# Kernel tuning notes

Hardware: AMD Instinct MI355X
Metric: run time of the kernel (lower is better)

## Reference

```python
import jax, jax.numpy as jnp
import numpy as np

B, S, N, H, C = 32, 128, 1024, 2, 128  # batch, seq_len(=in/out channels), num_nodes, heads, out_channels
NEG_SLOPE = 0.2


def setup_inputs() -> dict:
    key = jax.random.key(0)
    k1, k2, k3, k4 = jax.random.split(key, 4)
    scale = 1.0 / np.sqrt(S)
    return {
        "x": jax.random.normal(k1, (B, S, N), dtype=jnp.float32),
        "W": jax.random.normal(k2, (H, S, C), dtype=jnp.float32) * scale,
        "att_src": jax.random.normal(k3, (H, C), dtype=jnp.float32) * scale,
        "att_dst": jax.random.normal(k4, (H, C), dtype=jnp.float32) * scale,
        "bias": jnp.zeros((C,), dtype=jnp.float32),
    }


def reference(x, W, att_src, att_dst, bias):
    # x: [B, S, N] -> node features [B, N, S]
    xt = jnp.transpose(x, (0, 2, 1))
    # per-head projection: z [B, H, N, C]
    z = jnp.einsum('bns,hsc->bhnc', xt, W)
    # scalar attention scores per node: [B, H, N]
    s_src = jnp.einsum('bhnc,hc->bhn', z, att_src)
    s_dst = jnp.einsum('bhnc,hc->bhn', z, att_dst)
    # complete graph: e[i, j] = leaky_relu(s_dst[i] + s_src[j]); softmax over sources j
    e = jax.nn.leaky_relu(s_dst[..., :, None] + s_src[..., None, :], NEG_SLOPE)
    alpha = jax.nn.softmax(e, axis=-1)  # [B, H, N, N]
    out = jnp.einsum('bhij,bhjc->bhic', alpha, z)  # [B, H, N, C]
    out = jnp.mean(out, axis=1) + bias  # concat=False -> mean over heads; [B, N, C]
    return jnp.transpose(out, (0, 2, 1))  # [B, C(=S), N]
```

## Files before the change

kernel.cpp:

```cpp
#include <hip/hip_runtime.h>
#include <hip/hip_bf16.h>
#include <math.h>

constexpr int B_ = 32, S_ = 128, N_ = 1024, H_ = 2, C_ = 128;
#define L2E_ 1.44269504088896340736f

typedef short  bf16x8 __attribute__((ext_vector_type(8)));
typedef float  f32x4  __attribute__((ext_vector_type(4)));
typedef ushort u16x8  __attribute__((ext_vector_type(8)));

__device__ __forceinline__ ushort f2bf(float f) {
    __hip_bfloat16 h = __float2bfloat16(f);
    return __builtin_bit_cast(ushort, h);
}
__device__ __forceinline__ float bfhi(ushort u) {
    return __builtin_bit_cast(float, (uint)u << 16);
}

__global__ __launch_bounds__(256)
void prep_kernel(const float* __restrict__ x, const float* __restrict__ W,
                 ushort* __restrict__ xth, ushort* __restrict__ xtl,
                 ushort* __restrict__ wth, ushort* __restrict__ wtl)
{
    __shared__ float sm[128 * 129];
    const int tid = threadIdx.x;
    const int bx = blockIdx.x;
    if (bx < 512) {
        const int b = bx >> 4, nb = (bx & 15) * 64;
        const float* xb = x + (size_t)b * S_ * N_;
#pragma unroll
        for (int it = 0; it < 32; ++it) {
            int e = it * 256 + tid;
            int s = e >> 6, n = e & 63;
            sm[s * 65 + n] = xb[(size_t)s * N_ + nb + n];
        }
        __syncthreads();
        const int n = tid >> 2, sc = (tid & 3) * 32;
        const size_t rowb = ((size_t)b * N_ + nb + n) * S_ + sc;
#pragma unroll
        for (int g = 0; g < 4; ++g) {
            u16x8 vh, vl;
#pragma unroll
            for (int e = 0; e < 8; ++e) {
                float v = sm[(sc + g * 8 + e) * 65 + n];
                ushort hh = f2bf(v);
                vh[e] = hh;
                vl[e] = f2bf(v - bfhi(hh));
            }
            *(u16x8*)&xth[rowb + g * 8] = vh;
            *(u16x8*)&xtl[rowb + g * 8] = vl;
        }
    } else {
        const int h = bx - 512;
        const float* Wh = W + (size_t)h * S_ * C_;
#pragma unroll
        for (int it = 0; it < 64; ++it) {
            int e = it * 256 + tid;
            int s = e >> 7, c = e & 127;
            sm[s * 129 + c] = Wh[s * C_ + c];
        }
        __syncthreads();
        const int c = tid >> 1, sh = (tid & 1) * 64;
        const size_t rowb = ((size_t)h * C_ + c) * S_ + sh;
#pragma unroll
        for (int g = 0; g < 8; ++g) {
            u16x8 vh, vl;
#pragma unroll
            for (int e = 0; e < 8; ++e) {
                float v = sm[(sh + g * 8 + e) * 129 + c];
                ushort hh = f2bf(v);
                vh[e] = hh;
                vl[e] = f2bf(v - bfhi(hh));
            }
            *(u16x8*)&wth[rowb + g * 8] = vh;
            *(u16x8*)&wtl[rowb + g * 8] = vl;
        }
    }
}

__global__ __launch_bounds__(256, 2)
void proj_kernel(const ushort* __restrict__ xth, const ushort* __restrict__ xtl,
                 const ushort* __restrict__ wth, const ushort* __restrict__ wtl,
                 const float* __restrict__ att_src, const float* __restrict__ att_dst,
                 ushort* __restrict__ zt, float* __restrict__ ssrc,
                 float* __restrict__ sdst)
{
    const int nb = blockIdx.x * 64;
    const int bh = blockIdx.y;
    const int b = bh >> 1, h = bh & 1;
    const int w = threadIdx.x >> 6, lane = threadIdx.x & 63;
    const int lrow = lane & 15, lq = lane >> 4;

    f32x4 acc[8];
#pragma unroll
    for (int ct = 0; ct < 8; ++ct)
#pragma unroll
        for (int r = 0; r < 4; ++r) acc[ct][r] = 0.f;

    const size_t xrow = ((size_t)b * N_ + nb + w * 16 + lrow) * S_ + lq * 8;
    const size_t wbase = (size_t)h * C_ * S_ + (size_t)lrow * S_ + lq * 8;

#pragma unroll
    for (int kc = 0; kc < 4; ++kc) {
        bf16x8 ah = *(const bf16x8*)(xth + xrow + kc * 32);
        bf16x8 al = *(const bf16x8*)(xtl + xrow + kc * 32);
#pragma unroll
        for (int ct = 0; ct < 8; ++ct) {
            const size_t wo = wbase + (size_t)ct * 16 * S_ + kc * 32;
            bf16x8 bh8 = *(const bf16x8*)(wth + wo);
            bf16x8 bl8 = *(const bf16x8*)(wtl + wo);
            acc[ct] = __builtin_amdgcn_mfma_f32_16x16x32_bf16(ah, bh8, acc[ct], 0, 0, 0);
            acc[ct] = __builtin_amdgcn_mfma_f32_16x16x32_bf16(ah, bl8, acc[ct], 0, 0, 0);
            acc[ct] = __builtin_amdgcn_mfma_f32_16x16x32_bf16(al, bh8, acc[ct], 0, 0, 0);
        }
    }

    float asrc[8], adst[8];
#pragma unroll
    for (int ct = 0; ct < 8; ++ct) {
        asrc[ct] = att_src[h * C_ + ct * 16 + lrow];
        adst[ct] = att_dst[h * C_ + ct * 16 + lrow];
    }
#pragma unroll
    for (int r = 0; r < 4; ++r) {
        float ps = 0.f, pd = 0.f;
#pragma unroll
        for (int ct = 0; ct < 8; ++ct) {
            ps = fmaf(acc[ct][r], asrc[ct], ps);
            pd = fmaf(acc[ct][r], adst[ct], pd);
        }
#pragma unroll
        for (int msk = 8; msk >= 1; msk >>= 1) {
            ps += __shfl_xor(ps, msk, 64);
            pd += __shfl_xor(pd, msk, 64);
        }
        if (lrow == 0) {
            ssrc[(size_t)bh * N_ + nb + w * 16 + lq * 4 + r] = ps;
            sdst[(size_t)bh * N_ + nb + w * 16 + lq * 4 + r] = pd;
        }
    }

#pragma unroll
    for (int ct = 0; ct < 8; ++ct) {
        ushort4 v;
        v.x = f2bf(acc[ct][0]); v.y = f2bf(acc[ct][1]);
        v.z = f2bf(acc[ct][2]); v.w = f2bf(acc[ct][3]);
        *(ushort4*)&zt[((size_t)bh * C_ + ct * 16 + lrow) * N_ + nb + w * 16 + lq * 4] = v;
    }
}

__global__ __launch_bounds__(256)
void lsum_kernel(const float* __restrict__ ssrc, const float* __restrict__ sdst,
                 float* __restrict__ caA, float* __restrict__ cbA)
{
    const int bh = blockIdx.y, ib = blockIdx.x * 256;
    const int tid = threadIdx.x;
    __shared__ float sj[N_];
    __shared__ float red[4];

    float pm = -1e30f;
#pragma unroll
    for (int it = 0; it < 4; ++it) {
        int j = it * 256 + tid;
        float v = ssrc[(size_t)bh * N_ + j] * L2E_;
        sj[j] = v;
        pm = fmaxf(pm, v);
    }
#pragma unroll
    for (int msk = 1; msk < 64; msk <<= 1) pm = fmaxf(pm, __shfl_xor(pm, msk, 64));
    if ((tid & 63) == 0) red[tid >> 6] = pm;
    __syncthreads();
    const float smax = fmaxf(fmaxf(red[0], red[1]), fmaxf(red[2], red[3]));

    const float dt = sdst[(size_t)bh * N_ + ib + tid] * L2E_;
    const float vm = dt + smax;
    const float mt = fmaxf(vm, 0.2f * vm);
    const float c1 = dt - mt, c2 = 0.2f * dt - mt;

    float l0 = 0.f, l1 = 0.f, l2 = 0.f, l3 = 0.f;
    for (int j = 0; j < N_; j += 4) {
        float4 s4 = *(const float4*)&sj[j];
        l0 += exp2f(fmaxf(s4.x + c1, fmaf(0.2f, s4.x, c2)));
        l1 += exp2f(fmaxf(s4.y + c1, fmaf(0.2f, s4.y, c2)));
        l2 += exp2f(fmaxf(s4.z + c1, fmaf(0.2f, s4.z, c2)));
        l3 += exp2f(fmaxf(s4.w + c1, fmaf(0.2f, s4.w, c2)));
    }
    const float q = log2f((l0 + l1) + (l2 + l3));
    caA[(size_t)bh * N_ + ib + tid] = c1 - q;
    cbA[(size_t)bh * N_ + ib + tid] = c2 - q;
}

__device__ __forceinline__ void stage_chunk(const ushort* __restrict__ zt, uint* zstage,
                                            int b, int w, int lane, int buf, int j0)
{
#pragma unroll
    for (int it = 0; it < 8; ++it) {
        int id = (w * 8 + it) * 64 + lane;
        int hh = id >> 10, c = (id >> 3) & 127, jq = id & 7;
        const uint* src = (const uint*)(zt + (((size_t)(b * 2 + hh) * C_ + c) * N_)
                                       + j0 + ((jq ^ (c & 7)) << 3));
        __builtin_amdgcn_global_load_lds(
            (const __attribute__((address_space(1))) uint*)src,
            (__attribute__((address_space(3))) uint*)&zstage[buf * 8192 + (w * 8 + it) * 256],
            16, 0, 0);
    }
}

__global__ __launch_bounds__(256, 1)
void attn_kernel(const ushort* __restrict__ zt, const float* __restrict__ ssrc,
                 const float* __restrict__ caA, const float* __restrict__ cbA,
                 const float* __restrict__ bias, float* __restrict__ out)
{
    const int bx = blockIdx.x;
    const int b  = blockIdx.y;
    const int tid = threadIdx.x;
    const int w = tid >> 6, lane = tid & 63;
    const int rg = w >> 1, h = w & 1;
    const int lrow = lane & 15, lq = lane >> 4;
    const int rowbase = bx * 128 + rg * 64;
    const size_t bh = (size_t)b * 2 + h;

    __shared__ uint  zstage[16384];
    __shared__ float ssjl[2][N_];

    float ca[4], cb[4], bv[8];
#pragma unroll
    for (int t = 0; t < 4; ++t) {
        ca[t] = caA[bh * N_ + rowbase + t * 16 + lrow];
        cb[t] = cbA[bh * N_ + rowbase + t * 16 + lrow];
    }
#pragma unroll
    for (int ct = 0; ct < 8; ++ct) bv[ct] = bias[ct * 16 + lrow];

#pragma unroll
    for (int it = 0; it < 8; ++it) {
        int e = it * 256 + tid;
        int hh = e >> 10, j = e & 1023;
        ssjl[hh][j] = ssrc[((size_t)b * 2 + hh) * N_ + j] * L2E_;
    }

    stage_chunk(zt, zstage, b, w, lane, 0, 0);
    __syncthreads();

    f32x4 acc[4][8];
#pragma unroll
    for (int t = 0; t < 4; ++t)
#pragma unroll
        for (int ct = 0; ct < 8; ++ct)
#pragma unroll
            for (int r = 0; r < 4; ++r) acc[t][ct][r] = 0.f;

    int buf = 0;
    for (int jc = 0; jc < 16; ++jc) {
        if (jc < 15) stage_chunk(zt, zstage, b, w, lane, buf ^ 1, (jc + 1) * 64);
#pragma unroll
        for (int ks = 0; ks < 2; ++ks) {
            const int j32 = jc * 64 + ks * 32;
            bf16x8 bf[8];
#pragma unroll
            for (int ct = 0; ct < 8; ++ct) {
                int c = ct * 16 + lrow;
                int off = buf * 32768 + h * 16384 + c * 128 + ((((ks * 4) + lq) ^ (c & 7)) << 4);
                bf[ct] = *(const bf16x8*)((const char*)zstage + off);
            }
            float4 s0 = *(const float4*)&ssjl[h][j32 + lq * 8];
            float4 s1 = *(const float4*)&ssjl[h][j32 + lq * 8 + 4];
            float sv[8] = {s0.x, s0.y, s0.z, s0.w, s1.x, s1.y, s1.z, s1.w};
#pragma unroll
            for (int t = 0; t < 4; ++t) {
                bf16x8 af;
#pragma unroll
                for (int r = 0; r < 8; ++r) {
                    float e1 = fmaxf(sv[r] + ca[t], fmaf(0.2f, sv[r], cb[t]));
                    af[r] = (short)f2bf(exp2f(e1));
                }
#pragma unroll
                for (int ct = 0; ct < 8; ++ct)
                    acc[t][ct] = __builtin_amdgcn_mfma_f32_16x16x32_bf16(af, bf[ct], acc[t][ct], 0, 0, 0);
            }
        }
        __syncthreads();
        buf ^= 1;
    }

    float* exch = (float*)zstage;
    if (h == 1) {
#pragma unroll
        for (int t = 0; t < 4; ++t)
#pragma unroll
            for (int ct = 0; ct < 8; ++ct) {
                int idx = ((((rg * 4 + t) * 8 + ct) * 16 + lrow) * 16) + lq * 4;
                *(float4*)&exch[idx] = *(float4*)&acc[t][ct];
            }
    }
    __syncthreads();
    if (h == 0) {
#pragma unroll
        for (int t = 0; t < 4; ++t)
#pragma unroll
            for (int ct = 0; ct < 8; ++ct) {
                int idx = ((((rg * 4 + t) * 8 + ct) * 16 + lrow) * 16) + lq * 4;
                float4 v = *(const float4*)&exch[idx];
                int c = ct * 16 + lrow;
                float4 o;
                o.x = 0.5f * (acc[t][ct][0] + v.x) + bv[ct];
                o.y = 0.5f * (acc[t][ct][1] + v.y) + bv[ct];
                o.z = 0.5f * (acc[t][ct][2] + v.z) + bv[ct];
                o.w = 0.5f * (acc[t][ct][3] + v.w) + bv[ct];
                *(float4*)&out[((size_t)b * C_ + c) * N_ + rowbase + t * 16 + lq * 4] = o;
            }
    }
}

extern "C" void kernel_launch(void* const* d_in, const int* in_sizes, int n_in,
                              void* d_out, int out_size, void* d_ws, size_t ws_size,
                              hipStream_t stream) {
    const float* x       = (const float*)d_in[0];
    const float* W       = (const float*)d_in[1];
    const float* att_src = (const float*)d_in[2];
    const float* att_dst = (const float*)d_in[3];
    const float* bias    = (const float*)d_in[4];
    float* out = (float*)d_out;

    ushort* xth = (ushort*)d_ws;
    ushort* xtl = xth + (size_t)B_ * N_ * S_;
    ushort* wth = xtl + (size_t)B_ * N_ * S_;
    ushort* wtl = wth + (size_t)H_ * C_ * S_;
    ushort* zt  = wtl + (size_t)H_ * C_ * S_;
    float* ssrc = (float*)(zt + (size_t)B_ * H_ * C_ * N_);
    float* sdst = ssrc + (size_t)B_ * H_ * N_;
    float* caA  = sdst + (size_t)B_ * H_ * N_;
    float* cbA  = caA + (size_t)B_ * H_ * N_;

    prep_kernel<<<dim3(514), 256, 0, stream>>>(x, W, xth, xtl, wth, wtl);
    proj_kernel<<<dim3(N_ / 64, B_ * H_), 256, 0, stream>>>(
        xth, xtl, wth, wtl, att_src, att_dst, zt, ssrc, sdst);
    lsum_kernel<<<dim3(4, B_ * H_), 256, 0, stream>>>(ssrc, sdst, caA, cbA);
    attn_kernel<<<dim3(8, B_), 256, 0, stream>>>(zt, ssrc, caA, cbA, bias, out);
}
```

Baseline: 200.6 us.

## Factor softmax exponentials, fuse x conversion into projection, restructure attention blocks

The leaky-relu softmax is rewritten so that exp(leaky(d+s)) becomes a product of precomputed per-node exponentials, selected by a threshold compare. This removes the per-element exp2 from both the row-sum loop and the attention inner loop. The x split-bf16 transpose pass is folded into the projection kernel, which now reads fp32 x directly and handles both heads per block; only W keeps a separate prep kernel. The attention kernel moves to 512 threads with a split over source columns, an XCD-aware block mapping, and a multi-wave LDS reduction before a coalesced output store. The threshold products skip max subtraction and so risk overflow or underflow for large scores.

```diff
diff --git a/kernel.cpp b/kernel.cpp
--- a/kernel.cpp
+++ b/kernel.cpp
@@ -17,229 +17,226 @@
     return __builtin_bit_cast(float, (uint)u << 16);
 }
 
-__global__ __launch_bounds__(256)
-void prep_kernel(const float* __restrict__ x, const float* __restrict__ W,
-                 ushort* __restrict__ xth, ushort* __restrict__ xtl,
-                 ushort* __restrict__ wth, ushort* __restrict__ wtl)
+__global__ __launch_bounds__(512)
+void wprep_kernel(const float* __restrict__ W,
+                  ushort* __restrict__ wth, ushort* __restrict__ wtl)
 {
     __shared__ float sm[128 * 129];
-    const int tid = threadIdx.x;
-    const int bx = blockIdx.x;
-    if (bx < 512) {
-        const int b = bx >> 4, nb = (bx & 15) * 64;
-        const float* xb = x + (size_t)b * S_ * N_;
-#pragma unroll
-        for (int it = 0; it < 32; ++it) {
-            int e = it * 256 + tid;
-            int s = e >> 6, n = e & 63;
-            sm[s * 65 + n] = xb[(size_t)s * N_ + nb + n];
-        }
-        __syncthreads();
-        const int n = tid >> 2, sc = (tid & 3) * 32;
-        const size_t rowb = ((size_t)b * N_ + nb + n) * S_ + sc;
-#pragma unroll
-        for (int g = 0; g < 4; ++g) {
-            u16x8 vh, vl;
-#pragma unroll
-            for (int e = 0; e < 8; ++e) {
-                float v = sm[(sc + g * 8 + e) * 65 + n];
-                ushort hh = f2bf(v);
-                vh[e] = hh;
-                vl[e] = f2bf(v - bfhi(hh));
-            }
-            *(u16x8*)&xth[rowb + g * 8] = vh;
-            *(u16x8*)&xtl[rowb + g * 8] = vl;
-        }
-    } else {
-        const int h = bx - 512;
-        const float* Wh = W + (size_t)h * S_ * C_;
-#pragma unroll
-        for (int it = 0; it < 64; ++it) {
-            int e = it * 256 + tid;
-            int s = e >> 7, c = e & 127;
-            sm[s * 129 + c] = Wh[s * C_ + c];
-        }
-        __syncthreads();
-        const int c = tid >> 1, sh = (tid & 1) * 64;
-        const size_t rowb = ((size_t)h * C_ + c) * S_ + sh;
-#pragma unroll
-        for (int g = 0; g < 8; ++g) {
-            u16x8 vh, vl;
-#pragma unroll
-            for (int e = 0; e < 8; ++e) {
-                float v = sm[(sh + g * 8 + e) * 129 + c];
-                ushort hh = f2bf(v);
-                vh[e] = hh;
-                vl[e] = f2bf(v - bfhi(hh));
-            }
-            *(u16x8*)&wth[rowb + g * 8] = vh;
-            *(u16x8*)&wtl[rowb + g * 8] = vl;
-        }
-    }
-}
-
-__global__ __launch_bounds__(256, 2)
-void proj_kernel(const ushort* __restrict__ xth, const ushort* __restrict__ xtl,
+    const int h = blockIdx.x, tid = threadIdx.x;
+    const float* Wh = W + (size_t)h * S_ * C_;
+#pragma unroll
+    for (int it = 0; it < 32; ++it) {
+        int e = it * 512 + tid;
+        int s = e >> 7, c = e & 127;
+        sm[s * 129 + c] = Wh[e];
+    }
+    __syncthreads();
+    const int c = tid >> 2, sg = (tid & 3) * 32;
+    const size_t rowb = ((size_t)h * C_ + c) * S_ + sg;
+#pragma unroll
+    for (int g = 0; g < 4; ++g) {
+        u16x8 vh, vl;
+#pragma unroll
+        for (int e = 0; e < 8; ++e) {
+            float v = sm[(sg + g * 8 + e) * 129 + c];
+            ushort hh = f2bf(v);
+            vh[e] = hh;
+            vl[e] = f2bf(v - bfhi(hh));
+        }
+        *(u16x8*)&wth[rowb + g * 8] = vh;
+        *(u16x8*)&wtl[rowb + g * 8] = vl;
+    }
+}
+
+__global__ __launch_bounds__(512, 2)
+void proj_kernel(const float* __restrict__ x,
                  const ushort* __restrict__ wth, const ushort* __restrict__ wtl,
                  const float* __restrict__ att_src, const float* __restrict__ att_dst,
                  ushort* __restrict__ zt, float* __restrict__ ssrc,
                  float* __restrict__ sdst)
 {
-    const int nb = blockIdx.x * 64;
-    const int bh = blockIdx.y;
-    const int b = bh >> 1, h = bh & 1;
+    const int nb = blockIdx.x * 128;
+    const int b  = blockIdx.y;
     const int w = threadIdx.x >> 6, lane = threadIdx.x & 63;
+    const int wn = w >> 1, wh = w & 1;
     const int lrow = lane & 15, lq = lane >> 4;
-
-    f32x4 acc[8];
-#pragma unroll
-    for (int ct = 0; ct < 8; ++ct)
-#pragma unroll
-        for (int r = 0; r < 4; ++r) acc[ct][r] = 0.f;
-
-    const size_t xrow = ((size_t)b * N_ + nb + w * 16 + lrow) * S_ + lq * 8;
-    const size_t wbase = (size_t)h * C_ * S_ + (size_t)lrow * S_ + lq * 8;
+    const size_t bh = (size_t)(b * 2 + wh);
+
+    f32x4 acc[2][8];
+#pragma unroll
+    for (int tt = 0; tt < 2; ++tt)
+#pragma unroll
+        for (int ct = 0; ct < 8; ++ct)
+#pragma unroll
+            for (int r = 0; r < 4; ++r) acc[tt][ct][r] = 0.f;
+
+    const float* xp0 = x + (size_t)b * S_ * N_ + nb + wn * 32 + lrow;
+    const size_t wbase = (size_t)wh * C_ * S_ + (size_t)lrow * S_ + lq * 8;
 
 #pragma unroll
     for (int kc = 0; kc < 4; ++kc) {
-        bf16x8 ah = *(const bf16x8*)(xth + xrow + kc * 32);
-        bf16x8 al = *(const bf16x8*)(xtl + xrow + kc * 32);
+        bf16x8 ah[2], al[2];
+#pragma unroll
+        for (int tt = 0; tt < 2; ++tt) {
+            const float* xp = xp0 + tt * 16 + (size_t)(kc * 32 + lq * 8) * N_;
+#pragma unroll
+            for (int e = 0; e < 8; ++e) {
+                float v = xp[(size_t)e * N_];
+                ushort hi = f2bf(v);
+                ah[tt][e] = (short)hi;
+                al[tt][e] = (short)f2bf(v - bfhi(hi));
+            }
+        }
 #pragma unroll
         for (int ct = 0; ct < 8; ++ct) {
             const size_t wo = wbase + (size_t)ct * 16 * S_ + kc * 32;
-            bf16x8 bh8 = *(const bf16x8*)(wth + wo);
-            bf16x8 bl8 = *(const bf16x8*)(wtl + wo);
-            acc[ct] = __builtin_amdgcn_mfma_f32_16x16x32_bf16(ah, bh8, acc[ct], 0, 0, 0);
-            acc[ct] = __builtin_amdgcn_mfma_f32_16x16x32_bf16(ah, bl8, acc[ct], 0, 0, 0);
-            acc[ct] = __builtin_amdgcn_mfma_f32_16x16x32_bf16(al, bh8, acc[ct], 0, 0, 0);
+            bf16x8 bhv = *(const bf16x8*)(wth + wo);
+            bf16x8 blv = *(const bf16x8*)(wtl + wo);
+#pragma unroll
+            for (int tt = 0; tt < 2; ++tt) {
+                acc[tt][ct] = __builtin_amdgcn_mfma_f32_16x16x32_bf16(ah[tt], bhv, acc[tt][ct], 0, 0, 0);
+                acc[tt][ct] = __builtin_amdgcn_mfma_f32_16x16x32_bf16(ah[tt], blv, acc[tt][ct], 0, 0, 0);
+                acc[tt][ct] = __builtin_amdgcn_mfma_f32_16x16x32_bf16(al[tt], bhv, acc[tt][ct], 0, 0, 0);
+            }
         }
     }
 
     float asrc[8], adst[8];
 #pragma unroll
     for (int ct = 0; ct < 8; ++ct) {
-        asrc[ct] = att_src[h * C_ + ct * 16 + lrow];
-        adst[ct] = att_dst[h * C_ + ct * 16 + lrow];
-    }
-#pragma unroll
-    for (int r = 0; r < 4; ++r) {
-        float ps = 0.f, pd = 0.f;
+        asrc[ct] = att_src[wh * C_ + ct * 16 + lrow];
+        adst[ct] = att_dst[wh * C_ + ct * 16 + lrow];
+    }
+#pragma unroll
+    for (int tt = 0; tt < 2; ++tt)
+#pragma unroll
+        for (int r = 0; r < 4; ++r) {
+            float ps = 0.f, pd = 0.f;
+#pragma unroll
+            for (int ct = 0; ct < 8; ++ct) {
+                ps = fmaf(acc[tt][ct][r], asrc[ct], ps);
+                pd = fmaf(acc[tt][ct][r], adst[ct], pd);
+            }
+#pragma unroll
+            for (int msk = 8; msk >= 1; msk >>= 1) {
+                ps += __shfl_xor(ps, msk, 64);
+                pd += __shfl_xor(pd, msk, 64);
+            }
+            if (lrow == 0) {
+                int n = nb + wn * 32 + tt * 16 + lq * 4 + r;
+                ssrc[bh * N_ + n] = ps;
+                sdst[bh * N_ + n] = pd;
+            }
+        }
+
+#pragma unroll
+    for (int tt = 0; tt < 2; ++tt)
 #pragma unroll
         for (int ct = 0; ct < 8; ++ct) {
-            ps = fmaf(acc[ct][r], asrc[ct], ps);
-            pd = fmaf(acc[ct][r], adst[ct], pd);
-        }
-#pragma unroll
-        for (int msk = 8; msk >= 1; msk >>= 1) {
-            ps += __shfl_xor(ps, msk, 64);
-            pd += __shfl_xor(pd, msk, 64);
-        }
-        if (lrow == 0) {
-            ssrc[(size_t)bh * N_ + nb + w * 16 + lq * 4 + r] = ps;
-            sdst[(size_t)bh * N_ + nb + w * 16 + lq * 4 + r] = pd;
-        }
-    }
-
-#pragma unroll
-    for (int ct = 0; ct < 8; ++ct) {
-        ushort4 v;
-        v.x = f2bf(acc[ct][0]); v.y = f2bf(acc[ct][1]);
-        v.z = f2bf(acc[ct][2]); v.w = f2bf(acc[ct][3]);
-        *(ushort4*)&zt[((size_t)bh * C_ + ct * 16 + lrow) * N_ + nb + w * 16 + lq * 4] = v;
-    }
+            ushort4 v;
+            v.x = f2bf(acc[tt][ct][0]); v.y = f2bf(acc[tt][ct][1]);
+            v.z = f2bf(acc[tt][ct][2]); v.w = f2bf(acc[tt][ct][3]);
+            *(ushort4*)&zt[(bh * C_ + ct * 16 + lrow) * N_ + nb + wn * 32 + tt * 16 + lq * 4] = v;
+        }
 }
 
 __global__ __launch_bounds__(256)
 void lsum_kernel(const float* __restrict__ ssrc, const float* __restrict__ sdst,
-                 float* __restrict__ caA, float* __restrict__ cbA)
+                 float* __restrict__ e1t, float* __restrict__ e2t,
+                 float* __restrict__ Aar, float* __restrict__ Bar,
+                 float* __restrict__ Trar)
 {
     const int bh = blockIdx.y, ib = blockIdx.x * 256;
     const int tid = threadIdx.x;
-    __shared__ float sj[N_];
-    __shared__ float red[4];
-
-    float pm = -1e30f;
+    __shared__ float e1s[N_], e2s[N_];
+
 #pragma unroll
     for (int it = 0; it < 4; ++it) {
         int j = it * 256 + tid;
-        float v = ssrc[(size_t)bh * N_ + j] * L2E_;
-        sj[j] = v;
-        pm = fmaxf(pm, v);
-    }
-#pragma unroll
-    for (int msk = 1; msk < 64; msk <<= 1) pm = fmaxf(pm, __shfl_xor(pm, msk, 64));
-    if ((tid & 63) == 0) red[tid >> 6] = pm;
+        float sv = ssrc[(size_t)bh * N_ + j] * L2E_;
+        e1s[j] = exp2f(sv);
+        e2s[j] = exp2f(0.2f * sv);
+    }
     __syncthreads();
-    const float smax = fmaxf(fmaxf(red[0], red[1]), fmaxf(red[2], red[3]));
-
-    const float dt = sdst[(size_t)bh * N_ + ib + tid] * L2E_;
-    const float vm = dt + smax;
-    const float mt = fmaxf(vm, 0.2f * vm);
-    const float c1 = dt - mt, c2 = 0.2f * dt - mt;
+
+    const int i = ib + tid;
+    e1t[(size_t)bh * N_ + i] = e1s[i];
+    e2t[(size_t)bh * N_ + i] = e2s[i];
+
+    const float dt = sdst[(size_t)bh * N_ + i] * L2E_;
+    const float pA = exp2f(dt), pB = exp2f(0.2f * dt), Tr = exp2f(-dt);
 
     float l0 = 0.f, l1 = 0.f, l2 = 0.f, l3 = 0.f;
     for (int j = 0; j < N_; j += 4) {
-        float4 s4 = *(const float4*)&sj[j];
-        l0 += exp2f(fmaxf(s4.x + c1, fmaf(0.2f, s4.x, c2)));
-        l1 += exp2f(fmaxf(s4.y + c1, fmaf(0.2f, s4.y, c2)));
-        l2 += exp2f(fmaxf(s4.z + c1, fmaf(0.2f, s4.z, c2)));
-        l3 += exp2f(fmaxf(s4.w + c1, fmaf(0.2f, s4.w, c2)));
-    }
-    const float q = log2f((l0 + l1) + (l2 + l3));
-    caA[(size_t)bh * N_ + ib + tid] = c1 - q;
-    cbA[(size_t)bh * N_ + ib + tid] = c2 - q;
-}
-
-__device__ __forceinline__ void stage_chunk(const ushort* __restrict__ zt, uint* zstage,
-                                            int b, int w, int lane, int buf, int j0)
-{
-#pragma unroll
-    for (int it = 0; it < 8; ++it) {
-        int id = (w * 8 + it) * 64 + lane;
+        float a0 = e1s[j],     a1 = e1s[j + 1], a2 = e1s[j + 2], a3 = e1s[j + 3];
+        float b0 = e2s[j],     b1 = e2s[j + 1], b2 = e2s[j + 2], b3 = e2s[j + 3];
+        l0 += (a0 >= Tr) ? pA * a0 : pB * b0;
+        l1 += (a1 >= Tr) ? pA * a1 : pB * b1;
+        l2 += (a2 >= Tr) ? pA * a2 : pB * b2;
+        l3 += (a3 >= Tr) ? pA * a3 : pB * b3;
+    }
+    const float inv = 0.5f / ((l0 + l1) + (l2 + l3));
+    Aar[(size_t)bh * N_ + i]  = pA * inv;
+    Bar[(size_t)bh * N_ + i]  = pB * inv;
+    Trar[(size_t)bh * N_ + i] = Tr;
+}
+
+__device__ __forceinline__ void stage_chunk512(const ushort* __restrict__ zt,
+                                               uint* zstage, int b, int w,
+                                               int lane, int buf, int j0)
+{
+#pragma unroll
+    for (int it = 0; it < 4; ++it) {
+        int id = (w * 4 + it) * 64 + lane;
         int hh = id >> 10, c = (id >> 3) & 127, jq = id & 7;
         const uint* src = (const uint*)(zt + (((size_t)(b * 2 + hh) * C_ + c) * N_)
                                        + j0 + ((jq ^ (c & 7)) << 3));
         __builtin_amdgcn_global_load_lds(
             (const __attribute__((address_space(1))) uint*)src,
-            (__attribute__((address_space(3))) uint*)&zstage[buf * 8192 + (w * 8 + it) * 256],
+            (__attribute__((address_space(3))) uint*)&zstage[buf * 8192 + (w * 4 + it) * 256],
             16, 0, 0);
     }
 }
 
-__global__ __launch_bounds__(256, 1)
-void attn_kernel(const ushort* __restrict__ zt, const float* __restrict__ ssrc,
-                 const float* __restrict__ caA, const float* __restrict__ cbA,
-                 const float* __restrict__ bias, float* __restrict__ out)
-{
-    const int bx = blockIdx.x;
-    const int b  = blockIdx.y;
+__global__ __launch_bounds__(512, 2)
+void attn_kernel(const ushort* __restrict__ zt,
+                 const float* __restrict__ e1t, const float* __restrict__ e2t,
+                 const float* __restrict__ Aar, const float* __restrict__ Bar,
+                 const float* __restrict__ Trar, const float* __restrict__ bias,
+                 float* __restrict__ out)
+{
+    const int id0 = blockIdx.x;
+    const int xcd = id0 & 7, k = id0 >> 3;
+    const int b = xcd * 4 + (k >> 3), bx = k & 7;
+
     const int tid = threadIdx.x;
     const int w = tid >> 6, lane = tid & 63;
-    const int rg = w >> 1, h = w & 1;
+    const int rg = w >> 2, h = (w >> 1) & 1, js = w & 1;
     const int lrow = lane & 15, lq = lane >> 4;
     const int rowbase = bx * 128 + rg * 64;
-    const size_t bh = (size_t)b * 2 + h;
-
-    __shared__ uint  zstage[16384];
-    __shared__ float ssjl[2][N_];
-
-    float ca[4], cb[4], bv[8];
+    const size_t bh = (size_t)(b * 2 + h);
+
+    __shared__ char pool[128 * 132 * 4];
+    __shared__ float e1s[2][N_], e2s[2][N_];
+    uint* zstage = (uint*)pool;
+    float* exch  = (float*)pool;
+
+    float A4[4], B4[4], T4[4];
 #pragma unroll
     for (int t = 0; t < 4; ++t) {
-        ca[t] = caA[bh * N_ + rowbase + t * 16 + lrow];
-        cb[t] = cbA[bh * N_ + rowbase + t * 16 + lrow];
-    }
-#pragma unroll
-    for (int ct = 0; ct < 8; ++ct) bv[ct] = bias[ct * 16 + lrow];
-
-#pragma unroll
-    for (int it = 0; it < 8; ++it) {
-        int e = it * 256 + tid;
+        int i = rowbase + t * 16 + lrow;
+        A4[t] = Aar[bh * N_ + i];
+        B4[t] = Bar[bh * N_ + i];
+        T4[t] = Trar[bh * N_ + i];
+    }
+#pragma unroll
+    for (int it = 0; it < 4; ++it) {
+        int e = it * 512 + tid;
         int hh = e >> 10, j = e & 1023;
-        ssjl[hh][j] = ssrc[((size_t)b * 2 + hh) * N_ + j] * L2E_;
-    }
-
-    stage_chunk(zt, zstage, b, w, lane, 0, 0);
+        e1s[hh][j] = e1t[((size_t)b * 2 + hh) * N_ + j];
+        e2s[hh][j] = e2t[((size_t)b * 2 + hh) * N_ + j];
+    }
+    stage_chunk512(zt, zstage, b, w, lane, 0, 0);
     __syncthreads();
 
     f32x4 acc[4][8];
@@ -252,63 +249,72 @@
 
     int buf = 0;
     for (int jc = 0; jc < 16; ++jc) {
-        if (jc < 15) stage_chunk(zt, zstage, b, w, lane, buf ^ 1, (jc + 1) * 64);
-#pragma unroll
-        for (int ks = 0; ks < 2; ++ks) {
-            const int j32 = jc * 64 + ks * 32;
-            bf16x8 bf[8];
-#pragma unroll
-            for (int ct = 0; ct < 8; ++ct) {
-                int c = ct * 16 + lrow;
-                int off = buf * 32768 + h * 16384 + c * 128 + ((((ks * 4) + lq) ^ (c & 7)) << 4);
-                bf[ct] = *(const bf16x8*)((const char*)zstage + off);
-            }
-            float4 s0 = *(const float4*)&ssjl[h][j32 + lq * 8];
-            float4 s1 = *(const float4*)&ssjl[h][j32 + lq * 8 + 4];
-            float sv[8] = {s0.x, s0.y, s0.z, s0.w, s1.x, s1.y, s1.z, s1.w};
-#pragma unroll
-            for (int t = 0; t < 4; ++t) {
-                bf16x8 af;
-#pragma unroll
-                for (int r = 0; r < 8; ++r) {
-                    float e1 = fmaxf(sv[r] + ca[t], fmaf(0.2f, sv[r], cb[t]));
-                    af[r] = (short)f2bf(exp2f(e1));
-                }
-#pragma unroll
-                for (int ct = 0; ct < 8; ++ct)
-                    acc[t][ct] = __builtin_amdgcn_mfma_f32_16x16x32_bf16(af, bf[ct], acc[t][ct], 0, 0, 0);
-            }
+        if (jc < 15) stage_chunk512(zt, zstage, b, w, lane, buf ^ 1, (jc + 1) * 64);
+        const int j32 = jc * 64 + js * 32;
+
+        float4 e1a = *(const float4*)&e1s[h][j32 + lq * 8];
+        float4 e1b = *(const float4*)&e1s[h][j32 + lq * 8 + 4];
+        float4 e2a = *(const float4*)&e2s[h][j32 + lq * 8];
+        float4 e2b = *(const float4*)&e2s[h][j32 + lq * 8 + 4];
+        float ev1[8] = {e1a.x, e1a.y, e1a.z, e1a.w, e1b.x, e1b.y, e1b.z, e1b.w};
+        float ev2[8] = {e2a.x, e2a.y, e2a.z, e2a.w, e2b.x, e2b.y, e2b.z, e2b.w};
+
+        bf16x8 bf[8];
+#pragma unroll
+        for (int ct = 0; ct < 8; ++ct) {
+            int c = ct * 16 + lrow;
+            int off = buf * 32768 + h * 16384 + c * 128 + ((((js * 4) + lq) ^ (c & 7)) << 4);
+            bf[ct] = *(const bf16x8*)((const char*)zstage + off);
+        }
+#pragma unroll
+        for (int t = 0; t < 4; ++t) {
+            bf16x8 af;
+#pragma unroll
+            for (int r = 0; r < 8; ++r) {
+                float al = (ev1[r] >= T4[t]) ? A4[t] * ev1[r] : B4[t] * ev2[r];
+                af[r] = (short)f2bf(al);
+            }
+#pragma unroll
+            for (int ct = 0; ct < 8; ++ct)
+                acc[t][ct] = __builtin_amdgcn_mfma_f32_16x16x32_bf16(af, bf[ct], acc[t][ct], 0, 0, 0);
         }
         __syncthreads();
         buf ^= 1;
     }
 
-    float* exch = (float*)zstage;
-    if (h == 1) {
-#pragma unroll
-        for (int t = 0; t < 4; ++t)
-#pragma unroll
-            for (int ct = 0; ct < 8; ++ct) {
-                int idx = ((((rg * 4 + t) * 8 + ct) * 16 + lrow) * 16) + lq * 4;
-                *(float4*)&exch[idx] = *(float4*)&acc[t][ct];
-            }
-    }
-    __syncthreads();
-    if (h == 0) {
-#pragma unroll
-        for (int t = 0; t < 4; ++t)
-#pragma unroll
-            for (int ct = 0; ct < 8; ++ct) {
-                int idx = ((((rg * 4 + t) * 8 + ct) * 16 + lrow) * 16) + lq * 4;
-                float4 v = *(const float4*)&exch[idx];
-                int c = ct * 16 + lrow;
-                float4 o;
-                o.x = 0.5f * (acc[t][ct][0] + v.x) + bv[ct];
-                o.y = 0.5f * (acc[t][ct][1] + v.y) + bv[ct];
-                o.z = 0.5f * (acc[t][ct][2] + v.z) + bv[ct];
-                o.w = 0.5f * (acc[t][ct][3] + v.w) + bv[ct];
-                *(float4*)&out[((size_t)b * C_ + c) * N_ + rowbase + t * 16 + lq * 4] = o;
-            }
+    const int grp = w & 3;
+#pragma unroll 1
+    for (int p = 0; p < 4; ++p) {
+        if (grp == p) {
+#pragma unroll
+            for (int t = 0; t < 4; ++t)
+#pragma unroll
+                for (int ct = 0; ct < 8; ++ct) {
+                    int c = ct * 16 + lrow;
+                    int i = rg * 64 + t * 16 + lq * 4;
+                    float* dst = &exch[c * 132 + i];
+                    if (p == 0) {
+                        *(float4*)dst = make_float4(acc[t][ct][0], acc[t][ct][1],
+                                                    acc[t][ct][2], acc[t][ct][3]);
+                    } else {
+                        float4 v = *(const float4*)dst;
+                        v.x += acc[t][ct][0]; v.y += acc[t][ct][1];
+                        v.z += acc[t][ct][2]; v.w += acc[t][ct][3];
+                        *(float4*)dst = v;
+                    }
+                }
+        }
+        __syncthreads();
+    }
+
+    const int cl = tid >> 5, il = (tid & 31) * 4;
+#pragma unroll
+    for (int it = 0; it < 8; ++it) {
+        int c = it * 16 + cl;
+        float bvv = bias[c];
+        float4 v = *(const float4*)&exch[c * 132 + il];
+        v.x += bvv; v.y += bvv; v.z += bvv; v.w += bvv;
+        *(float4*)&out[((size_t)b * C_ + c) * N_ + bx * 128 + il] = v;
     }
 }
 
@@ -322,19 +328,22 @@
     const float* bias    = (const float*)d_in[4];
     float* out = (float*)d_out;
 
-    ushort* xth = (ushort*)d_ws;
-    ushort* xtl = xth + (size_t)B_ * N_ * S_;
-    ushort* wth = xtl + (size_t)B_ * N_ * S_;
+    ushort* wth = (ushort*)d_ws;
     ushort* wtl = wth + (size_t)H_ * C_ * S_;
     ushort* zt  = wtl + (size_t)H_ * C_ * S_;
     float* ssrc = (float*)(zt + (size_t)B_ * H_ * C_ * N_);
     float* sdst = ssrc + (size_t)B_ * H_ * N_;
-    float* caA  = sdst + (size_t)B_ * H_ * N_;
-    float* cbA  = caA + (size_t)B_ * H_ * N_;
-
-    prep_kernel<<<dim3(514), 256, 0, stream>>>(x, W, xth, xtl, wth, wtl);
-    proj_kernel<<<dim3(N_ / 64, B_ * H_), 256, 0, stream>>>(
-        xth, xtl, wth, wtl, att_src, att_dst, zt, ssrc, sdst);
-    lsum_kernel<<<dim3(4, B_ * H_), 256, 0, stream>>>(ssrc, sdst, caA, cbA);
-    attn_kernel<<<dim3(8, B_), 256, 0, stream>>>(zt, ssrc, caA, cbA, bias, out);
-}
+    float* e1t  = sdst + (size_t)B_ * H_ * N_;
+    float* e2t  = e1t + (size_t)B_ * H_ * N_;
+    float* Aar  = e2t + (size_t)B_ * H_ * N_;
+    float* Bar  = Aar + (size_t)B_ * H_ * N_;
+    float* Trar = Bar + (size_t)B_ * H_ * N_;
+
+    wprep_kernel<<<dim3(2), 512, 0, stream>>>(W, wth, wtl);
+    proj_kernel<<<dim3(8, 32), 512, 0, stream>>>(
+        x, wth, wtl, att_src, att_dst, zt, ssrc, sdst);
+    lsum_kernel<<<dim3(4, B_ * H_), 256, 0, stream>>>(
+        ssrc, sdst, e1t, e2t, Aar, Bar, Trar);
+    attn_kernel<<<dim3(256), 512, 0, stream>>>(
+        zt, e1t, e2t, Aar, Bar, Trar, bias, out);
+}
```

Measured after the change: 171.9 us. 1.17x faster.
